# Optimization experiments

Hardware: AMD Instinct MI355X
Metric: run time of the kernel (lower is better)

The kernel has to match this reference:

```python
import jax, jax.numpy as jnp
import numpy as np

EPS = 1e-5

def setup_inputs() -> dict:
    key = jax.random.key(0)
    k1, k2, k3 = jax.random.split(key, 3)
    B, T, F = 64, 512, 1024
    x = jax.random.normal(k1, (B, T, F), dtype=jnp.float32)
    # Linear(width_time, width_time): torch stores weight as (out, in)
    W = jax.random.normal(k2, (T, T), dtype=jnp.float32) * (1.0 / np.sqrt(T))
    b = jax.random.normal(k3, (T,), dtype=jnp.float32) * 0.01
    gamma = jnp.ones((1,), dtype=jnp.float32)
    beta = jnp.zeros((1,), dtype=jnp.float32)
    return {"x": x, "W": W, "b": b, "gamma": gamma, "beta": beta}


def reference(x, W, b, gamma, beta):
    # TSBatchNorm2d: BatchNorm2d(num_features=1) over x.unsqueeze(1)
    # -> stats over all (B, T, F) elements, scalar affine (training-mode batch stats).
    mean = jnp.mean(x)
    var = jnp.var(x)
    y = (x - mean) * jax.lax.rsqrt(var + EPS) * gamma[0] + beta[0]
    # transpose (B,T,F) -> (B,F,T), Linear over time dim, ReLU
    # (dropout is identity in eval mode), transpose back, residual add.
    yt = jnp.swapaxes(y, 1, 2)                      # (B, F, T)
    h = jnp.einsum('bft,ut->bfu', yt, W) + b        # Linear: y @ W.T + b
    h = jax.nn.relu(h)
    return x + jnp.swapaxes(h, 1, 2)                # (B, T, F)
```

## Files before the change

### kernel.cpp

```cpp
#include <hip/hip_runtime.h>
#include <stdint.h>

#define TDIM 512
#define FDIM 1024
#define NTOT 33554432.0f
#define EPS  1e-5f

typedef unsigned short ushort_t;
typedef unsigned short ushort4_t __attribute__((ext_vector_type(4)));
typedef short short8 __attribute__((ext_vector_type(8)));
typedef float floatx4 __attribute__((ext_vector_type(4)));

__device__ __forceinline__ ushort_t f2bf(float f) {
    union { float f; uint32_t u; } v; v.f = f;
    uint32_t r = (v.u + 0x7fffu + ((v.u >> 16) & 1u)) >> 16;
    return (ushort_t)r;
}

__device__ __forceinline__ void async16(const ushort_t* g, ushort_t* l) {
    __builtin_amdgcn_global_load_lds(
        (const __attribute__((address_space(1))) void*)g,
        (__attribute__((address_space(3))) void*)l, 16, 0, 0);
}


__global__ __launch_bounds__(256) void k_statsT(
    const float* __restrict__ x, const float* __restrict__ W,
    ushort_t* __restrict__ xTC, ushort_t* __restrict__ WbC,
    float* __restrict__ rowsumW, float2* __restrict__ partials)
{
    __shared__ ushort_t tile[64 * 128];
    __shared__ float red[8];

    int tid = threadIdx.x, bid = blockIdx.x;
    int lane = tid & 63, w = tid >> 6;

    if (bid >= 4096) {
        int u = bid - 4096;
        float2 lv = *(const float2*)(W + (size_t)u * 512 + 2 * tid);

        int mt = u >> 7, m = u & 127;
        int kt = tid >> 4;
        int qq = (tid & 15) >> 2;
        int e  = 2 * (tid & 3);
        size_t off = ((size_t)(mt * 16 + kt)) * 4096 + (size_t)(qq * 128 + m) * 8 + e;
        uint32_t pk = (uint32_t)f2bf(lv.x) | ((uint32_t)f2bf(lv.y) << 16);
        *(uint32_t*)&WbC[off] = pk;

        float s = lv.x + lv.y;
#pragma unroll
        for (int off2 = 32; off2 > 0; off2 >>= 1) s += __shfl_down(s, off2, 64);
        if (lane == 0) red[w] = s;
        __syncthreads();
        if (tid == 0) rowsumW[u] = red[0] + red[1] + red[2] + red[3];
        return;
    }

    int b  = bid >> 6;
    int t0 = ((bid >> 3) & 7) << 6;
    int ft = bid & 7;
    int f0 = ft << 7;

    int r8 = tid >> 5, c8 = tid & 31;
    const float* xb = x + ((size_t)(b * TDIM + t0) * FDIM) + f0;

    float4 v[8];
#pragma unroll
    for (int p = 0; p < 8; ++p)
        v[p] = *(const float4*)(xb + (size_t)(p * 8 + r8) * FDIM + c8 * 4);

    float s = 0.f, q = 0.f;
#pragma unroll
    for (int p = 0; p < 8; ++p) {
        float4 t = v[p];
        s += t.x + t.y + t.z + t.w;
        q += t.x * t.x + t.y * t.y + t.z * t.z + t.w * t.w;
        ushort4_t pk;
        pk[0] = f2bf(t.x); pk[1] = f2bf(t.y); pk[2] = f2bf(t.z); pk[3] = f2bf(t.w);
        *(ushort4_t*)&tile[(p * 8 + r8) * 128 + c8 * 4] = pk;
    }

#pragma unroll
    for (int off = 32; off > 0; off >>= 1) {
        s += __shfl_down(s, off, 64);
        q += __shfl_down(q, off, 64);
    }
    if (lane == 0) { red[w] = s; red[4 + w] = q; }
    __syncthreads();
    if (tid == 0) {
        partials[bid] = make_float2(red[0] + red[1] + red[2] + red[3],
                                    red[4] + red[5] + red[6] + red[7]);
    }

    int fl = tid & 127, hf = tid >> 7;
    size_t base = ((size_t)((b * 8 + ft) * 16) + (t0 >> 5) + hf) * 4096;
#pragma unroll
    for (int qq = 0; qq < 4; ++qq) {
        int tr = hf * 32 + qq * 8;
        uint32_t w0 = (uint32_t)tile[(tr + 0) * 128 + fl] | ((uint32_t)tile[(tr + 1) * 128 + fl] << 16);
        uint32_t w1 = (uint32_t)tile[(tr + 2) * 128 + fl] | ((uint32_t)tile[(tr + 3) * 128 + fl] << 16);
        uint32_t w2 = (uint32_t)tile[(tr + 4) * 128 + fl] | ((uint32_t)tile[(tr + 5) * 128 + fl] << 16);
        uint32_t w3 = (uint32_t)tile[(tr + 6) * 128 + fl] | ((uint32_t)tile[(tr + 7) * 128 + fl] << 16);
        uint4 o = make_uint4(w0, w1, w2, w3);
        *(uint4*)&xTC[base + (size_t)(qq * 128 + fl) * 8] = o;
    }
}

__global__ __launch_bounds__(256) void k_reduce(
    const float2* __restrict__ partials, const float* __restrict__ rowsumW,
    const float* __restrict__ bias, const float* __restrict__ gamma,
    const float* __restrict__ beta, float* __restrict__ stats,
    float* __restrict__ d)
{
    __shared__ float red[8];
    __shared__ float sac[2];
    int tid = threadIdx.x;
    float s = 0.f, q = 0.f;
#pragma unroll
    for (int i = 0; i < 16; ++i) {
        float2 p = partials[i * 256 + tid];
        s += p.x; q += p.y;
    }
#pragma unroll
    for (int off = 32; off > 0; off >>= 1) {
        s += __shfl_down(s, off, 64);
        q += __shfl_down(q, off, 64);
    }
    int lane = tid & 63, w = tid >> 6;
    if (lane == 0) { red[w] = s; red[4 + w] = q; }
    __syncthreads();
    if (tid == 0) {
        float S = red[0] + red[1] + red[2] + red[3];
        float Q = red[4] + red[5] + red[6] + red[7];
        float mean = S * (1.f / NTOT);
        float var  = Q * (1.f / NTOT) - mean * mean;
        float a    = gamma[0] * rsqrtf(var + EPS);
        float c    = beta[0] - mean * a;
        stats[0] = a;
        sac[0] = a; sac[1] = c;
    }
    __syncthreads();
    float c = sac[1];
    d[tid]       = c * rowsumW[tid]       + bias[tid];
    d[tid + 256] = c * rowsumW[tid + 256] + bias[tid + 256];
}

__global__ __launch_bounds__(256) void k_gemm(
    const ushort_t* __restrict__ WbC, const ushort_t* __restrict__ xTC,
    const float* __restrict__ x, const float* __restrict__ d,
    const float* __restrict__ stats, float* __restrict__ out)
{
    __shared__ ulong smem_raw[4096];
    ushort_t* lds  = (ushort_t*)smem_raw;
    float*    ldsC = (float*)smem_raw;

    int tid = threadIdx.x;
    int w = tid >> 6, lane = tid & 63;

    int hb   = blockIdx.x;
    int xcd  = hb & 7;
    int rr   = hb >> 3;
    int mt   = rr & 3;
    int nt   = ((rr >> 2) << 3) + xcd;
    int b = nt >> 3, ft = nt & 7;

    int wr = w >> 1, wc = w & 1;
    int l15 = lane & 15, q = lane >> 4;

    const ushort_t* Ab = WbC + (size_t)mt * 16 * 4096 + tid * 8;
    const ushort_t* Bb = xTC + (size_t)(b * 8 + ft) * 16 * 4096 + tid * 8;

    floatx4 acc[4][4] = {};

    auto stage = [&](int kt, int s) {
        const ushort_t* Ag = Ab + kt * 4096;
        const ushort_t* Bg = Bb + kt * 4096;
        ushort_t* ls = lds + s * 8192;
        async16(Ag,        &ls[tid * 8]);
        async16(Ag + 2048, &ls[2048 + tid * 8]);
        async16(Bg,        &ls[4096 + tid * 8]);
        async16(Bg + 2048, &ls[4096 + 2048 + tid * 8]);
    };

    stage(0, 0);

#pragma unroll
    for (int kt = 0; kt < 16; ++kt) {
        if (kt < 15) {
            stage(kt + 1, (kt + 1) & 1);
            asm volatile("s_waitcnt vmcnt(4)" ::: "memory");
        } else {
            asm volatile("s_waitcnt vmcnt(0)" ::: "memory");
        }
        __builtin_amdgcn_s_barrier();

        const ushort_t* cA = lds + (kt & 1) * 8192;
        const ushort_t* cB = cA + 4096;
        short8 af[4], bfr[4];
#pragma unroll
        for (int i = 0; i < 4; ++i) {
            int m = wr * 64 + i * 16 + l15;
            af[i] = *(const short8*)&cA[(q * 128 + m) * 8];
        }
#pragma unroll
        for (int j = 0; j < 4; ++j) {
            int n = wc * 64 + j * 16 + l15;
            bfr[j] = *(const short8*)&cB[(q * 128 + n) * 8];
        }
        asm volatile("s_waitcnt lgkmcnt(0)" ::: "memory");
        __builtin_amdgcn_s_barrier();

        __builtin_amdgcn_s_setprio(1);
#pragma unroll
        for (int i = 0; i < 4; ++i)
#pragma unroll
            for (int j = 0; j < 4; ++j)
                acc[i][j] = __builtin_amdgcn_mfma_f32_16x16x32_bf16(
                    af[i], bfr[j], acc[i][j], 0, 0, 0);
        __builtin_amdgcn_s_setprio(0);
    }

    __syncthreads();

    float a = stats[0];
    int row = tid >> 3, cs = (tid & 7) * 16;
#pragma unroll
    for (int p = 0; p < 4; ++p) {
        if (wr == (p >> 1)) {
#pragma unroll
            for (int ii = 0; ii < 2; ++ii) {
                int i = (p & 1) * 2 + ii;
                int rl0 = i * 16 + q * 4 - (p & 1) * 32;
#pragma unroll
                for (int j = 0; j < 4; ++j) {
                    int col = wc * 64 + j * 16 + l15;
#pragma unroll
                    for (int r = 0; r < 4; ++r)
                        ldsC[(rl0 + r) * 132 + col] = acc[i][j][r];
                }
            }
        }
        __syncthreads();
        int tg = mt * 128 + p * 32 + row;
        float dt = d[tg];
        size_t gbase = ((size_t)b * TDIM + tg) * FDIM + ft * 128 + cs;
        const float* xr = x + gbase;
        float* orow = out + gbase;
#pragma unroll
        for (int k4 = 0; k4 < 4; ++k4) {
            float4 xv = *(const float4*)(xr + k4 * 4);
            float4 cv = *(const float4*)&ldsC[row * 132 + cs + k4 * 4];
            float4 o;
            o.x = xv.x + fmaxf(a * cv.x + dt, 0.f);
            o.y = xv.y + fmaxf(a * cv.y + dt, 0.f);
            o.z = xv.z + fmaxf(a * cv.z + dt, 0.f);
            o.w = xv.w + fmaxf(a * cv.w + dt, 0.f);
            *(float4*)(orow + k4 * 4) = o;
        }
        __syncthreads();
    }
}

extern "C" void kernel_launch(void* const* d_in, const int* in_sizes, int n_in,
                              void* d_out, int out_size, void* d_ws, size_t ws_size,
                              hipStream_t stream) {
    const float* x     = (const float*)d_in[0];
    const float* W     = (const float*)d_in[1];
    const float* bias  = (const float*)d_in[2];
    const float* gamma = (const float*)d_in[3];
    const float* beta  = (const float*)d_in[4];
    float* out = (float*)d_out;

    char* ws = (char*)d_ws;
    float*    stats    = (float*)ws;
    float*    dvec     = (float*)(ws + 1024);
    float*    rowsumW  = (float*)(ws + 4096);
    float2*   partials = (float2*)(ws + 8192);
    ushort_t* WbC      = (ushort_t*)(ws + (64 << 10));
    ushort_t* xTC      = (ushort_t*)(ws + (1 << 20));

    k_statsT<<<4608, 256, 0, stream>>>(x, W, xTC, WbC, rowsumW, partials);
    k_reduce<<<1, 256, 0, stream>>>(partials, rowsumW, bias, gamma, beta, stats, dvec);
    k_gemm<<<2048, 256, 0, stream>>>(WbC, xTC, x, dvec, stats, out);
}
```

Measured before the change: 316.4 us.

## Triple-buffer LDS stages and overlap fragment loads with previous-step MFMAs

The GEMM main loop moves from double to triple LDS buffering, prefetching two k-tiles ahead with a looser vmcnt wait. Register fragments are double-buffered, so each iteration's MFMAs consume the previous step's fragments while the current step's LDS reads are in flight, and the final step is drained after the loop. This is meant to hide global-load and LDS-read latency behind matrix math. In exchange, LDS per block rises to 48KB and fragment register pressure doubles, which may lower occupancy, and the setprio hints are dropped.

```diff
diff --git a/kernel.cpp b/kernel.cpp
--- a/kernel.cpp
+++ b/kernel.cpp
@@ -150,7 +150,7 @@
     const float* __restrict__ x, const float* __restrict__ d,
     const float* __restrict__ stats, float* __restrict__ out)
 {
-    __shared__ ulong smem_raw[4096];
+    __shared__ ulong smem_raw[6144];
     ushort_t* lds  = (ushort_t*)smem_raw;
     float*    ldsC = (float*)smem_raw;
 
@@ -183,47 +183,61 @@
     };
 
     stage(0, 0);
+    stage(1, 1);
+
+    short8 af[2][4], bfr[2][4];
 
 #pragma unroll
     for (int kt = 0; kt < 16; ++kt) {
-        if (kt < 15) {
-            stage(kt + 1, (kt + 1) & 1);
+        if (kt < 14) {
+            stage(kt + 2, (kt + 2) % 3);
+            asm volatile("s_waitcnt vmcnt(8)" ::: "memory");
+        } else if (kt == 14) {
             asm volatile("s_waitcnt vmcnt(4)" ::: "memory");
         } else {
             asm volatile("s_waitcnt vmcnt(0)" ::: "memory");
         }
         __builtin_amdgcn_s_barrier();
 
-        const ushort_t* cA = lds + (kt & 1) * 8192;
+        const ushort_t* cA = lds + (kt % 3) * 8192;
         const ushort_t* cB = cA + 4096;
-        short8 af[4], bfr[4];
+        const int cs = kt & 1, ps = cs ^ 1;
+
 #pragma unroll
         for (int i = 0; i < 4; ++i) {
             int m = wr * 64 + i * 16 + l15;
-            af[i] = *(const short8*)&cA[(q * 128 + m) * 8];
+            af[cs][i] = *(const short8*)&cA[(q * 128 + m) * 8];
         }
 #pragma unroll
         for (int j = 0; j < 4; ++j) {
             int n = wc * 64 + j * 16 + l15;
-            bfr[j] = *(const short8*)&cB[(q * 128 + n) * 8];
-        }
+            bfr[cs][j] = *(const short8*)&cB[(q * 128 + n) * 8];
+        }
+
+        if (kt > 0) {
+#pragma unroll
+            for (int i = 0; i < 4; ++i)
+#pragma unroll
+                for (int j = 0; j < 4; ++j)
+                    acc[i][j] = __builtin_amdgcn_mfma_f32_16x16x32_bf16(
+                        af[ps][i], bfr[ps][j], acc[i][j], 0, 0, 0);
+        }
+
         asm volatile("s_waitcnt lgkmcnt(0)" ::: "memory");
         __builtin_amdgcn_s_barrier();
-
-        __builtin_amdgcn_s_setprio(1);
-#pragma unroll
-        for (int i = 0; i < 4; ++i)
-#pragma unroll
-            for (int j = 0; j < 4; ++j)
-                acc[i][j] = __builtin_amdgcn_mfma_f32_16x16x32_bf16(
-                    af[i], bfr[j], acc[i][j], 0, 0, 0);
-        __builtin_amdgcn_s_setprio(0);
-    }
+    }
+
+#pragma unroll
+    for (int i = 0; i < 4; ++i)
+#pragma unroll
+        for (int j = 0; j < 4; ++j)
+            acc[i][j] = __builtin_amdgcn_mfma_f32_16x16x32_bf16(
+                af[1][i], bfr[1][j], acc[i][j], 0, 0, 0);
 
     __syncthreads();
 
     float a = stats[0];
-    int row = tid >> 3, cs = (tid & 7) * 16;
+    int row = tid >> 3, cs2 = (tid & 7) * 16;
 #pragma unroll
     for (int p = 0; p < 4; ++p) {
         if (wr == (p >> 1)) {
@@ -243,13 +257,13 @@
         __syncthreads();
         int tg = mt * 128 + p * 32 + row;
         float dt = d[tg];
-        size_t gbase = ((size_t)b * TDIM + tg) * FDIM + ft * 128 + cs;
+        size_t gbase = ((size_t)b * TDIM + tg) * FDIM + ft * 128 + cs2;
         const float* xr = x + gbase;
         float* orow = out + gbase;
 #pragma unroll
         for (int k4 = 0; k4 < 4; ++k4) {
             float4 xv = *(const float4*)(xr + k4 * 4);
-            float4 cv = *(const float4*)&ldsC[row * 132 + cs + k4 * 4];
+            float4 cv = *(const float4*)&ldsC[row * 132 + cs2 + k4 * 4];
             float4 o;
             o.x = xv.x + fmaxf(a * cv.x + dt, 0.f);
             o.y = xv.y + fmaxf(a * cv.y + dt, 0.f);
```

Measured after the change: 310.5 us. No clear change (-1.9%).
